# Performance work log

Measured on AMD Instinct MI355X. Metric: run time of the kernel, lower is better.

The kernel has to match this reference:

```python
import jax, jax.numpy as jnp
import numpy as np

EPS = 1e-8

def _center_gram(g):
    # H @ g @ H with H = I - 11^T/n  ==  double mean-centering (same math, O(n^2))
    row_mean = g.mean(axis=1, keepdims=True)   # (n,1)
    col_mean = g.mean(axis=0, keepdims=True)   # (1,n)
    grand = g.mean()
    return g - row_mean - col_mean + grand

def _hsic(a, b):
    K = _center_gram(a @ a.T)
    L = _center_gram(b @ b.T)
    return (K * L).sum()

def setup_inputs() -> dict:
    key = jax.random.key(0)
    k1, k2 = jax.random.split(key)
    x = jax.random.normal(k1, (8192, 2048), dtype=jnp.float32)
    y = jax.random.normal(k2, (8192, 1024), dtype=jnp.float32)
    return {"x": x, "y": y}

def reference(x, y):
    hsic_xy = _hsic(x, y)
    hsic_xx = _hsic(x, x)
    hsic_yy = _hsic(y, y)
    return hsic_xy / (jnp.sqrt(hsic_xx * hsic_yy) + EPS)
```

## Files before the change

kernel.cpp:

```cpp
#include <hip/hip_runtime.h>
#include <hip/hip_bf16.h>
#include <math.h>

typedef unsigned int uint;
typedef unsigned short ushort;
typedef __attribute__((ext_vector_type(4))) int i32x4;
typedef __attribute__((ext_vector_type(8))) ushort u16x8;

#define K_DIM 8192
#define ROW8 8192
#define N_TILE 300
#define S_SPLIT 3
#define NKT 64
#define QSC (127.0f / 6.0f)


__device__ __forceinline__ void async16(const void* g, void* l) {
  __builtin_amdgcn_global_load_lds(
      (const __attribute__((address_space(1))) unsigned int*)g,
      (__attribute__((address_space(3))) unsigned int*)l, 16, 0, 0);
}

__device__ __forceinline__ ushort f2bf(float f) {
  uint x = __float_as_uint(f);
  uint r = (x + 0x7fffu + ((x >> 16) & 1u)) >> 16;
  return (ushort)r;
}

__global__ __launch_bounds__(256) void zero_k(double* sums, double* dots) {
  int t = threadIdx.x;
  if (t < 4) sums[t] = 0.0;
  if (t >= 4 && t < 10) dots[t - 4] = 0.0;
}

__global__ __launch_bounds__(256) void quantT_k(const float* __restrict__ x,
                                                const float* __restrict__ y,
                                                char* XT8, char* YT8) {
  __shared__ float tile[64][129];
  int bid = blockIdx.x, t = threadIdx.x;
  const float* src; char* dst; int C, mt, kt;
  if (bid < 2048) { src = x; dst = XT8; C = 2048; mt = bid >> 6; kt = bid & 63; }
  else { int b = bid - 2048; src = y; dst = YT8; C = 1024; mt = b >> 6; kt = b & 63; }
  int m0 = mt * 64, k0 = kt * 128;

#pragma unroll
  for (int rep = 0; rep < 32; rep++) {
    int idx = rep * 256 + t;
    int kr = idx >> 6, mc = idx & 63;
    tile[mc][kr] = src[(size_t)(k0 + kr) * C + (size_t)(m0 + mc)];
  }
  __syncthreads();

  int u3 = t & 7, mlb = t >> 3;
#pragma unroll
  for (int rep2 = 0; rep2 < 2; rep2++) {
    int ml = mlb + rep2 * 32;
    int m = m0 + ml;
    uint wd[4];
#pragma unroll
    for (int jw = 0; jw < 4; jw++) {
      uint wv = 0;
#pragma unroll
      for (int b = 0; b < 4; b++) {
        float f = tile[ml][u3 * 16 + jw * 4 + b] * QSC;
        int qv = __float2int_rn(f);
        qv = max(-127, min(127, qv));
        wv |= ((uint)(qv & 0xFF)) << (8 * b);
      }
      wd[jw] = wv;
    }
    size_t off = (size_t)m * ROW8 + (size_t)k0 + (size_t)(u3 * 16);
    uint4 v; v.x = wd[0]; v.y = wd[1]; v.z = wd[2]; v.w = wd[3];
    *(uint4*)(dst + off) = v;
  }
}

__global__ __launch_bounds__(256) void rowstat_k(const char* __restrict__ XT8,
                                                 const char* __restrict__ YT8,
                                                 int* __restrict__ Rg,
                                                 float* __restrict__ upart,
                                                 double* dots) {
  __shared__ int pr[4];
  int bid = blockIdx.x, t = threadIdx.x, w = t >> 6, lane = t & 63;
  const char* src; int rbase, dslot;
  if (bid < 64) { src = XT8 + (size_t)bid * 32 * ROW8; rbase = bid * 32; dslot = 0; }
  else { src = YT8 + (size_t)(bid - 64) * 32 * ROW8; rbase = 2048 + (bid - 64) * 32; dslot = 1; }

  float acc[32];
#pragma unroll
  for (int c = 0; c < 32; c++) acc[c] = 0.f;
  double r2 = 0.0;

  for (int row = 0; row < 32; row++) {
    const int* p = (const int*)(src + (size_t)row * ROW8 + t * 32);
    int wds[8];
#pragma unroll
    for (int j = 0; j < 8; j++) wds[j] = p[j];
    int s = 0;
#pragma unroll
    for (int j = 0; j < 8; j++)
#pragma unroll
      for (int b = 0; b < 4; b++) s += (int)(signed char)(wds[j] >> (8 * b));
    for (int off = 32; off; off >>= 1) s += __shfl_down(s, off, 64);
    if (lane == 0) pr[w] = s;
    __syncthreads();
    int R = pr[0] + pr[1] + pr[2] + pr[3];
    if (t == 0) { Rg[rbase + row] = R; r2 += (double)R * (double)R; }
    float rw = (float)R;
#pragma unroll
    for (int j = 0; j < 8; j++)
#pragma unroll
      for (int b = 0; b < 4; b++)
        acc[j * 4 + b] += rw * (float)(int)(signed char)(wds[j] >> (8 * b));
    __syncthreads();
  }

  float* up = upart + (size_t)bid * 8192 + t * 32;
#pragma unroll
  for (int j = 0; j < 8; j++) {
    float4 v; v.x = acc[j * 4]; v.y = acc[j * 4 + 1]; v.z = acc[j * 4 + 2]; v.w = acc[j * 4 + 3];
    *(float4*)(up + j * 4) = v;
  }
  if (t == 0) atomicAdd(&dots[dslot], r2);
}

__global__ __launch_bounds__(256) void dots_k(const float* __restrict__ upart,
                                              double* dots) {
  __shared__ double pd[4][3];
  int k = blockIdx.x * 256 + threadIdx.x;
  int t = threadIdx.x, w = t >> 6, lane = t & 63;
  float ux = 0.f, uy = 0.f;
#pragma unroll 8
  for (int b = 0; b < 64; b++) ux += upart[(size_t)b * 8192 + k];
#pragma unroll 8
  for (int b = 64; b < 96; b++) uy += upart[(size_t)b * 8192 + k];
  double dxy = (double)ux * (double)uy;
  double dx2 = (double)ux * (double)ux;
  double dy2 = (double)uy * (double)uy;
  for (int off = 32; off; off >>= 1) {
    dxy += __shfl_down(dxy, off, 64);
    dx2 += __shfl_down(dx2, off, 64);
    dy2 += __shfl_down(dy2, off, 64);
  }
  if (lane == 0) { pd[w][0] = dxy; pd[w][1] = dx2; pd[w][2] = dy2; }
  __syncthreads();
  if (t == 0) {
    atomicAdd(&dots[2], pd[0][0] + pd[1][0] + pd[2][0] + pd[3][0]);
    atomicAdd(&dots[3], pd[0][1] + pd[1][1] + pd[2][1] + pd[3][1]);
    atomicAdd(&dots[4], pd[0][2] + pd[1][2] + pd[2][2] + pd[3][2]);
  }
}

__device__ __forceinline__ void tile_decomp(int tile, int* m0, int* n0,
                                            int* which, int* diag) {
  if (tile < 128) { *m0 = (tile >> 3) * 128; *n0 = (tile & 7) * 128; *which = 0; *diag = 0; }
  else if (tile < 264) {
    int idx = tile - 128, ti = 0;
    while (idx >= 16 - ti) { idx -= 16 - ti; ti++; }
    *m0 = ti * 128; *n0 = (ti + idx) * 128; *which = 1; *diag = (idx == 0);
  } else {
    int idx = tile - 264, ti = 0;
    while (idx >= 8 - ti) { idx -= 8 - ti; ti++; }
    *m0 = ti * 128; *n0 = (ti + idx) * 128; *which = 2; *diag = (idx == 0);
  }
}

__global__ __launch_bounds__(256, 4) void gemm_i8_k(const char* __restrict__ XT8,
                                                    const char* __restrict__ YT8,
                                                    ushort* __restrict__ Cp) {
  __shared__ char lds[32768];

  int orig = blockIdx.x;
  int xcd = orig & 7, idx8 = orig >> 3;
  int off = (xcd < 4) ? xcd * 113 : 4 * 113 + (xcd - 4) * 112;
  int wgid = off + idx8;
  int s = wgid / N_TILE, tile = wgid - s * N_TILE;

  int m0, n0, which, diag;
  tile_decomp(tile, &m0, &n0, &which, &diag);
  const char* Ab = (which == 2) ? YT8 : XT8;
  const char* Bb = (which == 0) ? YT8 : (which == 1) ? XT8 : YT8;
  const char* Ag = Ab + (size_t)m0 * ROW8;
  const char* Bg = Bb + (size_t)n0 * ROW8;
  const float invs = (6.0f / 127.0f) * (6.0f / 127.0f);

  int k0t = (NKT * s) / S_SPLIT;
  int k1t = (NKT * (s + 1)) / S_SPLIT;
  int nst = k1t - k0t;

  int t = threadIdx.x;
  int u = t & 7;
  int rr = t >> 3;
  int w = t >> 6;
  int lane = t & 63;
  int wm = (w >> 1) * 64, wn = (w & 1) * 64;
  int lr = lane & 15, lk = lane >> 4;
  const bool doB = !diag;

  i32x4 acc[4][4];
#pragma unroll
  for (int i = 0; i < 4; i++)
#pragma unroll
    for (int j = 0; j < 4; j++)
      acc[i][j] = (i32x4){0, 0, 0, 0};

#define STAGE(kt)                                                                   \
  {                                                                                 \
    size_t koff = (size_t)(kt) * 128;                                               \
    _Pragma("unroll")                                                               \
    for (int c = 0; c < 4; c++) {                                                   \
      int row = c * 32 + rr;                                                        \
      size_t gsrc = (size_t)row * ROW8 + koff + (size_t)((u ^ (row & 7)) << 4);     \
      async16(Ag + gsrc, lds + row * 128 + u * 16);                                 \
      if (doB)                                                                      \
        async16(Bg + gsrc, lds + 16384 + row * 128 + u * 16);                       \
    }                                                                               \
  }

  for (int i = 0; i < nst; ++i) {
    __syncthreads();
    STAGE(k0t + i);
    __syncthreads();

    const char* la = lds;
    const char* lb = doB ? (lds + 16384) : lds;
#pragma unroll
    for (int ks = 0; ks < 2; ks++) {
      int ku = ks * 4 + lk;
      i32x4 a[4], b[4];
#pragma unroll
      for (int mi = 0; mi < 4; mi++) {
        int row = wm + mi * 16 + lr;
        a[mi] = *(const i32x4*)(la + row * 128 + ((ku ^ (row & 7)) << 4));
      }
#pragma unroll
      for (int nj = 0; nj < 4; nj++) {
        int row = wn + nj * 16 + lr;
        b[nj] = *(const i32x4*)(lb + row * 128 + ((ku ^ (row & 7)) << 4));
      }
#pragma unroll
      for (int mi = 0; mi < 4; mi++)
#pragma unroll
        for (int nj = 0; nj < 4; nj++)
          acc[mi][nj] = __builtin_amdgcn_mfma_i32_16x16x64_i8(a[mi], b[nj], acc[mi][nj], 0, 0, 0);
    }
  }
#undef STAGE

  ushort* Ct = Cp + (size_t)(tile * S_SPLIT + s) * 16384;
#pragma unroll
  for (int mi = 0; mi < 4; mi++)
#pragma unroll
    for (int nj = 0; nj < 4; nj++)
#pragma unroll
      for (int e = 0; e < 4; e++)
        Ct[w * 4096 + (mi * 4 + nj) * 256 + e * 64 + lane] =
            f2bf((float)acc[mi][nj][e] * invs);
}

__global__ __launch_bounds__(256) void reduceC_k(const ushort* __restrict__ Cp,
                                                 double* sums) {
  __shared__ double p[4];
  int tile = blockIdx.x, t = threadIdx.x;
  int m0, n0, which, diag;
  tile_decomp(tile, &m0, &n0, &which, &diag);
  double wgt = diag ? 1.0 : (which == 0 ? 1.0 : 2.0);

  const ushort* C0 = Cp + (size_t)(tile * S_SPLIT) * 16384;
  double s = 0.0;
#pragma unroll
  for (int v = 0; v < 8; v++) {
    int idx = t * 64 + v * 8;
    u16x8 a0 = *(const u16x8*)(C0 + idx);
    u16x8 a1 = *(const u16x8*)(C0 + 16384 + idx);
    u16x8 a2 = *(const u16x8*)(C0 + 32768 + idx);
#pragma unroll
    for (int j = 0; j < 8; j++) {
      float c = __uint_as_float((uint)a0[j] << 16) +
                __uint_as_float((uint)a1[j] << 16) +
                __uint_as_float((uint)a2[j] << 16);
      s += (double)(c * c);
    }
  }
  for (int off = 32; off; off >>= 1) s += __shfl_down(s, off, 64);
  if ((t & 63) == 0) p[t >> 6] = s;
  __syncthreads();
  if (t == 0) atomicAdd(&sums[which], wgt * (p[0] + p[1] + p[2] + p[3]));
}

__global__ void finalize_k(const double* sums, const double* dots, float* out) {
  const double n = 8192.0;
  const double invs = (6.0 / 127.0) * (6.0 / 127.0);
  const double i2 = invs * invs;
  double hxy = sums[0] - 2.0 * i2 * dots[2] / n + i2 * dots[0] * dots[1] / (n * n);
  double hxx = sums[1] - 2.0 * i2 * dots[3] / n + i2 * dots[0] * dots[0] / (n * n);
  double hyy = sums[2] - 2.0 * i2 * dots[4] / n + i2 * dots[1] * dots[1] / (n * n);
  out[0] = (float)(hxy / (sqrt(hxx * hyy) + 1e-8));
}

extern "C" void kernel_launch(void* const* d_in, const int* in_sizes, int n_in,
                              void* d_out, int out_size, void* d_ws, size_t ws_size,
                              hipStream_t stream) {
  (void)in_sizes; (void)n_in; (void)out_size; (void)ws_size;
  const float* x = (const float*)d_in[0];
  const float* y = (const float*)d_in[1];
  float* out = (float*)d_out;
  char* ws = (char*)d_ws;
  double* sums = (double*)ws;
  double* dots = (double*)(ws + 64);
  int* Rg = (int*)(ws + 128);
  float* upart = (float*)(ws + 16384);
  char* XT8 = ws + 4194304;
  char* YT8 = ws + 20971520;
  ushort* Cp = (ushort*)(ws + 29360128);

  zero_k<<<1, 256, 0, stream>>>(sums, dots);
  quantT_k<<<3072, 256, 0, stream>>>(x, y, XT8, YT8);
  rowstat_k<<<96, 256, 0, stream>>>(XT8, YT8, Rg, upart, dots);
  gemm_i8_k<<<N_TILE * S_SPLIT, 256, 0, stream>>>(XT8, YT8, Cp);
  reduceC_k<<<N_TILE, 256, 0, stream>>>(Cp, sums);
  dots_k<<<32, 256, 0, stream>>>(upart, dots);
  finalize_k<<<1, 1, 0, stream>>>(sums, dots, out);
}
```

Baseline: 125.4 us.

## Fuse row sums into quantization, parallelize u-pass, load GEMM B operand directly

Row sums of the quantized matrices are now accumulated inside the quantize/transpose kernel with shuffles and atomics. This replaces the serial rowstat kernel, which used two barriers per row, with a more parallel upass kernel that does integer accumulation. The GEMM K-split goes from 3 to 4 with a uniform split, only the A tile is staged through LDS, and the B fragments are read straight from global memory into registers. The intent is to cut synchronization-heavy preprocessing and halve LDS use, at the risk of uncoalesced global B loads with no latency hiding and more partial C traffic.

```diff
diff --git a/kernel.cpp b/kernel.cpp
--- a/kernel.cpp
+++ b/kernel.cpp
@@ -10,7 +10,7 @@
 #define K_DIM 8192
 #define ROW8 8192
 #define N_TILE 300
-#define S_SPLIT 3
+#define S_SPLIT 4
 #define NKT 64
 #define QSC (127.0f / 6.0f)
 
@@ -27,20 +27,22 @@
   return (ushort)r;
 }
 
-__global__ __launch_bounds__(256) void zero_k(double* sums, double* dots) {
+__global__ __launch_bounds__(256) void zero_k(double* sums, double* dots, int* Rg) {
   int t = threadIdx.x;
   if (t < 4) sums[t] = 0.0;
   if (t >= 4 && t < 10) dots[t - 4] = 0.0;
+  for (int i = t; i < 3072; i += 256) Rg[i] = 0;
 }
 
 __global__ __launch_bounds__(256) void quantT_k(const float* __restrict__ x,
                                                 const float* __restrict__ y,
-                                                char* XT8, char* YT8) {
+                                                char* XT8, char* YT8,
+                                                int* __restrict__ Rg) {
   __shared__ float tile[64][129];
   int bid = blockIdx.x, t = threadIdx.x;
-  const float* src; char* dst; int C, mt, kt;
-  if (bid < 2048) { src = x; dst = XT8; C = 2048; mt = bid >> 6; kt = bid & 63; }
-  else { int b = bid - 2048; src = y; dst = YT8; C = 1024; mt = b >> 6; kt = b & 63; }
+  const float* src; char* dst; int C, mt, kt, rgbase;
+  if (bid < 2048) { src = x; dst = XT8; C = 2048; mt = bid >> 6; kt = bid & 63; rgbase = 0; }
+  else { int b = bid - 2048; src = y; dst = YT8; C = 1024; mt = b >> 6; kt = b & 63; rgbase = 2048; }
   int m0 = mt * 64, k0 = kt * 128;
 
 #pragma unroll
@@ -57,6 +59,7 @@
     int ml = mlb + rep2 * 32;
     int m = m0 + ml;
     uint wd[4];
+    int rs = 0;
 #pragma unroll
     for (int jw = 0; jw < 4; jw++) {
       uint wv = 0;
@@ -65,6 +68,7 @@
         float f = tile[ml][u3 * 16 + jw * 4 + b] * QSC;
         int qv = __float2int_rn(f);
         qv = max(-127, min(127, qv));
+        rs += qv;
         wv |= ((uint)(qv & 0xFF)) << (8 * b);
       }
       wd[jw] = wv;
@@ -72,71 +76,57 @@
     size_t off = (size_t)m * ROW8 + (size_t)k0 + (size_t)(u3 * 16);
     uint4 v; v.x = wd[0]; v.y = wd[1]; v.z = wd[2]; v.w = wd[3];
     *(uint4*)(dst + off) = v;
-  }
-}
-
-__global__ __launch_bounds__(256) void rowstat_k(const char* __restrict__ XT8,
-                                                 const char* __restrict__ YT8,
-                                                 int* __restrict__ Rg,
-                                                 float* __restrict__ upart,
-                                                 double* dots) {
-  __shared__ int pr[4];
-  int bid = blockIdx.x, t = threadIdx.x, w = t >> 6, lane = t & 63;
-  const char* src; int rbase, dslot;
-  if (bid < 64) { src = XT8 + (size_t)bid * 32 * ROW8; rbase = bid * 32; dslot = 0; }
-  else { src = YT8 + (size_t)(bid - 64) * 32 * ROW8; rbase = 2048 + (bid - 64) * 32; dslot = 1; }
-
-  float acc[32];
-#pragma unroll
-  for (int c = 0; c < 32; c++) acc[c] = 0.f;
-  double r2 = 0.0;
-
-  for (int row = 0; row < 32; row++) {
-    const int* p = (const int*)(src + (size_t)row * ROW8 + t * 32);
-    int wds[8];
-#pragma unroll
-    for (int j = 0; j < 8; j++) wds[j] = p[j];
-    int s = 0;
-#pragma unroll
-    for (int j = 0; j < 8; j++)
-#pragma unroll
-      for (int b = 0; b < 4; b++) s += (int)(signed char)(wds[j] >> (8 * b));
-    for (int off = 32; off; off >>= 1) s += __shfl_down(s, off, 64);
-    if (lane == 0) pr[w] = s;
-    __syncthreads();
-    int R = pr[0] + pr[1] + pr[2] + pr[3];
-    if (t == 0) { Rg[rbase + row] = R; r2 += (double)R * (double)R; }
-    float rw = (float)R;
-#pragma unroll
-    for (int j = 0; j < 8; j++)
-#pragma unroll
-      for (int b = 0; b < 4; b++)
-        acc[j * 4 + b] += rw * (float)(int)(signed char)(wds[j] >> (8 * b));
-    __syncthreads();
-  }
-
-  float* up = upart + (size_t)bid * 8192 + t * 32;
-#pragma unroll
-  for (int j = 0; j < 8; j++) {
-    float4 v; v.x = acc[j * 4]; v.y = acc[j * 4 + 1]; v.z = acc[j * 4 + 2]; v.w = acc[j * 4 + 3];
-    *(float4*)(up + j * 4) = v;
-  }
-  if (t == 0) atomicAdd(&dots[dslot], r2);
-}
-
-__global__ __launch_bounds__(256) void dots_k(const float* __restrict__ upart,
-                                              double* dots) {
+    rs += __shfl_down(rs, 4, 8);
+    rs += __shfl_down(rs, 2, 8);
+    rs += __shfl_down(rs, 1, 8);
+    if (u3 == 0) atomicAdd(&Rg[rgbase + m], rs);
+  }
+}
+
+__global__ __launch_bounds__(256) void upass_k(const char* __restrict__ XT8,
+                                               const char* __restrict__ YT8,
+                                               const int* __restrict__ Rg,
+                                               int* __restrict__ upart,
+                                               double* dots) {
+  int bid = blockIdx.x, t = threadIdx.x;
+  const char* src; int rc, kc, rgbase, slot, dslot;
+  if (bid < 256) { rc = bid >> 3; kc = bid & 7; src = XT8; rgbase = 0; slot = rc; dslot = 0; }
+  else { int b = bid - 256; rc = b >> 3; kc = b & 7; src = YT8; rgbase = 2048; slot = 32 + rc; dslot = 1; }
+  int rbase = rc * 64;
+  size_t cbase = (size_t)kc * 1024 + (size_t)t * 4;
+
+  int a0 = 0, a1 = 0, a2 = 0, a3 = 0;
+#pragma unroll 8
+  for (int r = 0; r < 64; r++) {
+    int wv = *(const int*)(src + (size_t)(rbase + r) * ROW8 + cbase);
+    int R = Rg[rgbase + rbase + r];
+    a0 += R * (int)(signed char)(wv);
+    a1 += R * (int)(signed char)(wv >> 8);
+    a2 += R * (int)(signed char)(wv >> 16);
+    a3 += R * (int)(signed char)(wv >> 24);
+  }
+  int4 vo; vo.x = a0; vo.y = a1; vo.z = a2; vo.w = a3;
+  *(int4*)(upart + (size_t)slot * 8192 + kc * 1024 + t * 4) = vo;
+
+  if (kc == 0 && t < 64) {
+    double R = (double)Rg[rgbase + rbase + t];
+    double r2 = R * R;
+    for (int off = 32; off; off >>= 1) r2 += __shfl_down(r2, off, 64);
+    if (t == 0) atomicAdd(&dots[dslot], r2);
+  }
+}
+
+__global__ __launch_bounds__(256) void dots2_k(const int* __restrict__ upart,
+                                               double* dots) {
   __shared__ double pd[4][3];
   int k = blockIdx.x * 256 + threadIdx.x;
   int t = threadIdx.x, w = t >> 6, lane = t & 63;
-  float ux = 0.f, uy = 0.f;
-#pragma unroll 8
-  for (int b = 0; b < 64; b++) ux += upart[(size_t)b * 8192 + k];
-#pragma unroll 8
-  for (int b = 64; b < 96; b++) uy += upart[(size_t)b * 8192 + k];
-  double dxy = (double)ux * (double)uy;
-  double dx2 = (double)ux * (double)ux;
-  double dy2 = (double)uy * (double)uy;
+  double ux = 0.0, uy = 0.0;
+#pragma unroll
+  for (int b = 0; b < 32; b++) ux += (double)upart[(size_t)b * 8192 + k];
+#pragma unroll
+  for (int b = 32; b < 48; b++) uy += (double)upart[(size_t)b * 8192 + k];
+  double dxy = ux * uy, dx2 = ux * ux, dy2 = uy * uy;
   for (int off = 32; off; off >>= 1) {
     dxy += __shfl_down(dxy, off, 64);
     dx2 += __shfl_down(dx2, off, 64);
@@ -168,12 +158,11 @@
 __global__ __launch_bounds__(256, 4) void gemm_i8_k(const char* __restrict__ XT8,
                                                     const char* __restrict__ YT8,
                                                     ushort* __restrict__ Cp) {
-  __shared__ char lds[32768];
+  __shared__ char lds[16384];
 
   int orig = blockIdx.x;
   int xcd = orig & 7, idx8 = orig >> 3;
-  int off = (xcd < 4) ? xcd * 113 : 4 * 113 + (xcd - 4) * 112;
-  int wgid = off + idx8;
+  int wgid = xcd * 150 + idx8;
   int s = wgid / N_TILE, tile = wgid - s * N_TILE;
 
   int m0, n0, which, diag;
@@ -184,9 +173,7 @@
   const char* Bg = Bb + (size_t)n0 * ROW8;
   const float invs = (6.0f / 127.0f) * (6.0f / 127.0f);
 
-  int k0t = (NKT * s) / S_SPLIT;
-  int k1t = (NKT * (s + 1)) / S_SPLIT;
-  int nst = k1t - k0t;
+  int k0t = 16 * s;
 
   int t = threadIdx.x;
   int u = t & 7;
@@ -195,7 +182,11 @@
   int lane = t & 63;
   int wm = (w >> 1) * 64, wn = (w & 1) * 64;
   int lr = lane & 15, lk = lane >> 4;
-  const bool doB = !diag;
+
+  const char* Bl[4];
+#pragma unroll
+  for (int nj = 0; nj < 4; nj++)
+    Bl[nj] = Bg + (size_t)(wn + nj * 16 + lr) * ROW8 + (size_t)(lk * 16);
 
   i32x4 acc[4][4];
 #pragma unroll
@@ -204,7 +195,7 @@
     for (int j = 0; j < 4; j++)
       acc[i][j] = (i32x4){0, 0, 0, 0};
 
-#define STAGE(kt)                                                                   \
+#define STAGE_A(kt)                                                                 \
   {                                                                                 \
     size_t koff = (size_t)(kt) * 128;                                               \
     _Pragma("unroll")                                                               \
@@ -212,31 +203,26 @@
       int row = c * 32 + rr;                                                        \
       size_t gsrc = (size_t)row * ROW8 + koff + (size_t)((u ^ (row & 7)) << 4);     \
       async16(Ag + gsrc, lds + row * 128 + u * 16);                                 \
-      if (doB)                                                                      \
-        async16(Bg + gsrc, lds + 16384 + row * 128 + u * 16);                       \
     }                                                                               \
   }
 
-  for (int i = 0; i < nst; ++i) {
+  for (int i = 0; i < 16; ++i) {
     __syncthreads();
-    STAGE(k0t + i);
+    STAGE_A(k0t + i);
     __syncthreads();
 
-    const char* la = lds;
-    const char* lb = doB ? (lds + 16384) : lds;
+    size_t kb = (size_t)(k0t + i) * 128;
 #pragma unroll
     for (int ks = 0; ks < 2; ks++) {
       int ku = ks * 4 + lk;
       i32x4 a[4], b[4];
 #pragma unroll
+      for (int nj = 0; nj < 4; nj++)
+        b[nj] = *(const i32x4*)(Bl[nj] + kb + ks * 64);
+#pragma unroll
       for (int mi = 0; mi < 4; mi++) {
         int row = wm + mi * 16 + lr;
-        a[mi] = *(const i32x4*)(la + row * 128 + ((ku ^ (row & 7)) << 4));
-      }
-#pragma unroll
-      for (int nj = 0; nj < 4; nj++) {
-        int row = wn + nj * 16 + lr;
-        b[nj] = *(const i32x4*)(lb + row * 128 + ((ku ^ (row & 7)) << 4));
+        a[mi] = *(const i32x4*)(lds + row * 128 + ((ku ^ (row & 7)) << 4));
       }
 #pragma unroll
       for (int mi = 0; mi < 4; mi++)
@@ -245,7 +231,7 @@
           acc[mi][nj] = __builtin_amdgcn_mfma_i32_16x16x64_i8(a[mi], b[nj], acc[mi][nj], 0, 0, 0);
     }
   }
-#undef STAGE
+#undef STAGE_A
 
   ushort* Ct = Cp + (size_t)(tile * S_SPLIT + s) * 16384;
 #pragma unroll
@@ -274,11 +260,13 @@
     u16x8 a0 = *(const u16x8*)(C0 + idx);
     u16x8 a1 = *(const u16x8*)(C0 + 16384 + idx);
     u16x8 a2 = *(const u16x8*)(C0 + 32768 + idx);
+    u16x8 a3 = *(const u16x8*)(C0 + 49152 + idx);
 #pragma unroll
     for (int j = 0; j < 8; j++) {
       float c = __uint_as_float((uint)a0[j] << 16) +
                 __uint_as_float((uint)a1[j] << 16) +
-                __uint_as_float((uint)a2[j] << 16);
+                __uint_as_float((uint)a2[j] << 16) +
+                __uint_as_float((uint)a3[j] << 16);
       s += (double)(c * c);
     }
   }
@@ -309,16 +297,16 @@
   double* sums = (double*)ws;
   double* dots = (double*)(ws + 64);
   int* Rg = (int*)(ws + 128);
-  float* upart = (float*)(ws + 16384);
-  char* XT8 = ws + 4194304;
-  char* YT8 = ws + 20971520;
-  ushort* Cp = (ushort*)(ws + 29360128);
-
-  zero_k<<<1, 256, 0, stream>>>(sums, dots);
-  quantT_k<<<3072, 256, 0, stream>>>(x, y, XT8, YT8);
-  rowstat_k<<<96, 256, 0, stream>>>(XT8, YT8, Rg, upart, dots);
+  int* upart = (int*)(ws + 16384);
+  char* XT8 = ws + 2097152;
+  char* YT8 = ws + 18874368;
+  ushort* Cp = (ushort*)(ws + 27262976);
+
+  zero_k<<<1, 256, 0, stream>>>(sums, dots, Rg);
+  quantT_k<<<3072, 256, 0, stream>>>(x, y, XT8, YT8, Rg);
   gemm_i8_k<<<N_TILE * S_SPLIT, 256, 0, stream>>>(XT8, YT8, Cp);
+  upass_k<<<384, 256, 0, stream>>>(XT8, YT8, Rg, upart, dots);
   reduceC_k<<<N_TILE, 256, 0, stream>>>(Cp, sums);
-  dots_k<<<32, 256, 0, stream>>>(upart, dots);
+  dots2_k<<<32, 256, 0, stream>>>(upart, dots);
   finalize_k<<<1, 1, 0, stream>>>(sums, dots, out);
 }
```

Measured after the change: 171.4 us. +36.7%, slower.
